# Performance work log

Measured on AMD Instinct MI355X. Metric: run time of the kernel, lower is better.

The kernel has to match this reference:

```python
import jax, jax.numpy as jnp
import numpy as np

B, C, H, W, K = 2, 3, 256, 256, 51  # output H,W; filter size K; input is (H+K-1, W+K-1)


def _sepconv(inp, vertical, horizontal):
    # inp: [B,C,H+K-1,W+K-1]; vertical/horizontal: [B,K,H,W]
    Kf = vertical.shape[1]
    Ho, Wo = vertical.shape[2], vertical.shape[3]
    rows = jnp.stack([inp[:, :, i:i + Ho, :] for i in range(Kf)], axis=0)

    def body(acc, j):
        # window for horizontal offset j: [K,B,C,Ho,Wo]
        win = jax.lax.dynamic_slice_in_dim(rows, j, Wo, axis=4)
        # contract over vertical taps i with per-pixel vertical kernel
        vcon = jnp.einsum('kbchw,bkhw->bchw', win, vertical)
        # weight by per-pixel horizontal tap j and accumulate
        acc = acc + vcon * horizontal[:, j][:, None, :, :]
        return acc, None

    acc0 = jnp.zeros((inp.shape[0], inp.shape[1], Ho, Wo), inp.dtype)
    out, _ = jax.lax.scan(body, acc0, jnp.arange(Kf))
    return out


def setup_inputs() -> dict:
    key = jax.random.key(0)
    k1, k2, k3 = jax.random.split(key, 3)
    tenInput = jax.random.normal(k1, (B, C, H + K - 1, W + K - 1), dtype=jnp.float32)
    tenVertical = jax.random.normal(k2, (B, K, H, W), dtype=jnp.float32)
    tenHorizontal = jax.random.normal(k3, (B, K, H, W), dtype=jnp.float32)
    return {"tenInput": tenInput, "tenVertical": tenVertical, "tenHorizontal": tenHorizontal}


def reference(tenInput, tenVertical, tenHorizontal):
    return _sepconv(tenInput, tenVertical, tenHorizontal)
```

## Files before the change

kernel.cpp:

```cpp
#include <hip/hip_runtime.h>


namespace {
constexpr int KK = 51;
constexpr int NB = 2;
constexpr int NC = 3;
constexpr int HH = 256;
constexpr int WW = 256;
constexpr int IN_H = HH + KK - 1;
constexpr int IN_W = WW + KK - 1;

constexpr int TILE_W = 64;
constexpr int TILE_H = 8;
constexpr int NTX = 8;
constexpr int R = 8;
constexpr int NTY = 8;
constexpr int NS = 4;
constexpr int NTHREADS = NTX * NTY * NS;
constexpr int HALO_W = TILE_W + KK - 1;
constexpr int LDS_W = 116;
constexpr int LDS_H = TILE_H + KK - 1;
constexpr int KSTRIDE = HH * WW;
}

__device__ __forceinline__ float fget(const float4 v, int i) {
  return (i == 0) ? v.x : (i == 1) ? v.y : (i == 2) ? v.z : v.w;
}

template <int P, int JJ>
__device__ __forceinline__ void fma_jtap(const float4 (&v4)[4][2], const float4 (&w4)[4][3],
                                         const float4 ha, const float4 hb, float (&acc)[R]) {
#pragma unroll
  for (int rx = 0; rx < R; ++rx) {
    const int k  = rx + JJ;
    const int sl = (P + k / 4) % 3;
    const int cp = k & 3;
    const int vh = rx >> 2, vc = rx & 3;
    float tv = fget(v4[0][vh], vc) * fget(w4[0][sl], cp);
    tv = fmaf(fget(v4[1][vh], vc), fget(w4[1][sl], cp), tv);
    tv = fmaf(fget(v4[2][vh], vc), fget(w4[2][sl], cp), tv);
    tv = fmaf(fget(v4[3][vh], vc), fget(w4[3][sl], cp), tv);
    const float hv = (rx < 4) ? fget(ha, vc) : fget(hb, vc);
    acc[rx] = fmaf(hv, tv, acc[rx]);
  }
}

template <int P>
__device__ __forceinline__ void do_chunk(const float4 (&v4)[4][2], float4 (&w4)[4][3],
                                         const int (&woff)[4], int ldcol,
                                         const float* hp, float (&acc)[R],
                                         const float* smem) {
  const float4 h0a = *reinterpret_cast<const float4*>(hp);
  const float4 h0b = *reinterpret_cast<const float4*>(hp + 4);
  const float4 h1a = *reinterpret_cast<const float4*>(hp + KSTRIDE);
  const float4 h1b = *reinterpret_cast<const float4*>(hp + KSTRIDE + 4);
  fma_jtap<P, 0>(v4, w4, h0a, h0b, acc);
  const float4 h2a = *reinterpret_cast<const float4*>(hp + 2 * (size_t)KSTRIDE);
  const float4 h2b = *reinterpret_cast<const float4*>(hp + 2 * (size_t)KSTRIDE + 4);
  const float4 h3a = *reinterpret_cast<const float4*>(hp + 3 * (size_t)KSTRIDE);
  const float4 h3b = *reinterpret_cast<const float4*>(hp + 3 * (size_t)KSTRIDE + 4);
  fma_jtap<P, 1>(v4, w4, h1a, h1b, acc);
  fma_jtap<P, 2>(v4, w4, h2a, h2b, acc);
  fma_jtap<P, 3>(v4, w4, h3a, h3b, acc);
#pragma unroll
  for (int ib = 0; ib < 4; ++ib)
    w4[ib][P] = *reinterpret_cast<const float4*>(&smem[woff[ib] + ldcol]);
}

__global__ __launch_bounds__(NTHREADS, 1)
void sepconv_kernel(
    const float* __restrict__ inp,
    const float* __restrict__ vert,
    const float* __restrict__ horiz,
    float* __restrict__ out)
{
  __shared__ float lds[LDS_H * LDS_W];

  const int tid = threadIdx.x;
  const int tx  = tid & (NTX - 1);
  const int ty  = (tid >> 3) & (NTY - 1);
  const int s   = tid >> 6;

  const int x0 = blockIdx.x * TILE_W;
  const int y0 = blockIdx.y * TILE_H;
  const int bc = blockIdx.z;
  const int b  = bc / NC;
  const int c  = bc % NC;

  {
    const float* src = inp + (((size_t)(b * NC + c)) * IN_H + y0) * IN_W + x0;
    constexpr int total2 = LDS_H * (HALO_W / 2);
    for (int e = tid; e < total2; e += NTHREADS) {
      const int col2 = e % (HALO_W / 2);
      const int r    = e / (HALO_W / 2);
      const float2 v = *reinterpret_cast<const float2*>(src + (size_t)r * IN_W + col2 * 2);
      float* dst = &lds[r * LDS_W + col2 * 2];
      dst[0] = v.x; dst[1] = v.y;
    }
  }
  __syncthreads();

  const int lx = tx * R;
  const int xg = x0 + lx;
  const int yg = y0 + ty;

  float acc[R];
#pragma unroll
  for (int rx = 0; rx < R; ++rx) acc[rx] = 0.f;

  const int blk0 = (s == 0) ? 0 : (3 * s + 1);
  const int nblk = (s == 0) ? 4 : 3;

  const float* vbase = vert  + (((size_t)b * KK) * HH + yg) * WW + xg;
  const float* hbase = horiz + (((size_t)b * KK) * HH + yg) * WW + xg;

#pragma unroll 1
  for (int t = 0; t < nblk; ++t) {
    const int ibase = (blk0 + t) * 4;

    float4 v4[4][2];
    float4 w4[4][3];
    int    woff[4];
#pragma unroll
    for (int ib = 0; ib < 4; ++ib) {
      const int iv = ibase + ib;
      const int ic = (iv <= 50) ? iv : 50;
      float4 va = *reinterpret_cast<const float4*>(vbase + (size_t)ic * KSTRIDE);
      float4 vb = *reinterpret_cast<const float4*>(vbase + (size_t)ic * KSTRIDE + 4);
      if (iv > 50) { va = make_float4(0.f, 0.f, 0.f, 0.f); vb = va; }
      v4[ib][0] = va; v4[ib][1] = vb;
      woff[ib] = (ty + ic) * LDS_W;
      const float4* p = reinterpret_cast<const float4*>(&lds[woff[ib] + lx]);
      w4[ib][0] = p[0]; w4[ib][1] = p[1]; w4[ib][2] = p[2];
    }

    const float* hp = hbase;

#pragma unroll 1
    for (int cc = 0; cc < 4; ++cc) {
      const int base = lx + 12 * cc + 12;
      do_chunk<0>(v4, w4, woff, base + 0, hp, acc, lds); hp += 4 * (size_t)KSTRIDE;
      do_chunk<1>(v4, w4, woff, base + 4, hp, acc, lds); hp += 4 * (size_t)KSTRIDE;
      do_chunk<2>(v4, w4, woff, base + 8, hp, acc, lds); hp += 4 * (size_t)KSTRIDE;
    }

    {
      const float4 e0a = *reinterpret_cast<const float4*>(hp);
      const float4 e0b = *reinterpret_cast<const float4*>(hp + 4);
      const float4 e1a = *reinterpret_cast<const float4*>(hp + KSTRIDE);
      const float4 e1b = *reinterpret_cast<const float4*>(hp + KSTRIDE + 4);
      const float4 e2a = *reinterpret_cast<const float4*>(hp + 2 * (size_t)KSTRIDE);
      const float4 e2b = *reinterpret_cast<const float4*>(hp + 2 * (size_t)KSTRIDE + 4);
      fma_jtap<0, 0>(v4, w4, e0a, e0b, acc);
      fma_jtap<0, 1>(v4, w4, e1a, e1b, acc);
      fma_jtap<0, 2>(v4, w4, e2a, e2b, acc);
    }
  }

  __syncthreads();
  if (s > 0) {
    float* p = &lds[((s - 1) * 64 + ty * NTX + tx) * R];
#pragma unroll
    for (int rx = 0; rx < R; ++rx) p[rx] = acc[rx];
  }
  __syncthreads();
  if (s == 0) {
#pragma unroll
    for (int g = 0; g < 3; ++g) {
      const float* p = &lds[(g * 64 + ty * NTX + tx) * R];
#pragma unroll
      for (int rx = 0; rx < R; ++rx) acc[rx] += p[rx];
    }
    float* o = out + (((size_t)(b * NC + c)) * HH + yg) * WW + xg;
    *reinterpret_cast<float4*>(o)     = make_float4(acc[0], acc[1], acc[2], acc[3]);
    *reinterpret_cast<float4*>(o + 4) = make_float4(acc[4], acc[5], acc[6], acc[7]);
  }
}

extern "C" void kernel_launch(void* const* d_in, const int* in_sizes, int n_in,
                              void* d_out, int out_size, void* d_ws, size_t ws_size,
                              hipStream_t stream) {
  const float* inp   = (const float*)d_in[0];
  const float* vert  = (const float*)d_in[1];
  const float* horiz = (const float*)d_in[2];
  float* out = (float*)d_out;

  dim3 grid(WW / TILE_W, HH / TILE_H, NB * NC);
  sepconv_kernel<<<grid, NTHREADS, 0, stream>>>(inp, vert, horiz, out);
}
```

Measured before the change: 159.4 us.

## Stage horizontal taps into double-buffered LDS via async global_load_lds

Instead of each of the four split-groups reading the horizontal filter taps directly from global memory (each group redundantly), the block cooperatively stages 4 taps per step into a swizzled double-buffered LDS area using global_load_lds, then all groups read from LDS. This removes the 4x redundant global reads of the horizontal weights and overlaps the next chunk's load with compute. In exchange it adds a block-wide barrier per chunk, forces all groups to iterate 4 times even when only 3 are active, and increases LDS usage.

```diff
diff --git a/kernel.cpp b/kernel.cpp
--- a/kernel.cpp
+++ b/kernel.cpp
@@ -21,6 +21,7 @@
 constexpr int LDS_W = 116;
 constexpr int LDS_H = TILE_H + KK - 1;
 constexpr int KSTRIDE = HH * WW;
+constexpr int HCH = 4 * TILE_H * TILE_W;
 }
 
 __device__ __forceinline__ float fget(const float4 v, int i) {
@@ -46,25 +47,25 @@
 }
 
 template <int P>
-__device__ __forceinline__ void do_chunk(const float4 (&v4)[4][2], float4 (&w4)[4][3],
-                                         const int (&woff)[4], int ldcol,
-                                         const float* hp, float (&acc)[R],
-                                         const float* smem) {
-  const float4 h0a = *reinterpret_cast<const float4*>(hp);
-  const float4 h0b = *reinterpret_cast<const float4*>(hp + 4);
-  const float4 h1a = *reinterpret_cast<const float4*>(hp + KSTRIDE);
-  const float4 h1b = *reinterpret_cast<const float4*>(hp + KSTRIDE + 4);
+__device__ __forceinline__ void full_chunk(const float4 (&v4)[4][2], float4 (&w4)[4][3],
+                                           const int (&woff)[4], int wcol,
+                                           const float* hb, int off0, int off1,
+                                           float (&acc)[R], const float* smem) {
+  const float4 h0a = *reinterpret_cast<const float4*>(hb + off0);
+  const float4 h0b = *reinterpret_cast<const float4*>(hb + off1);
+  const float4 h1a = *reinterpret_cast<const float4*>(hb + 512 + off0);
+  const float4 h1b = *reinterpret_cast<const float4*>(hb + 512 + off1);
   fma_jtap<P, 0>(v4, w4, h0a, h0b, acc);
-  const float4 h2a = *reinterpret_cast<const float4*>(hp + 2 * (size_t)KSTRIDE);
-  const float4 h2b = *reinterpret_cast<const float4*>(hp + 2 * (size_t)KSTRIDE + 4);
-  const float4 h3a = *reinterpret_cast<const float4*>(hp + 3 * (size_t)KSTRIDE);
-  const float4 h3b = *reinterpret_cast<const float4*>(hp + 3 * (size_t)KSTRIDE + 4);
+  const float4 h2a = *reinterpret_cast<const float4*>(hb + 1024 + off0);
+  const float4 h2b = *reinterpret_cast<const float4*>(hb + 1024 + off1);
   fma_jtap<P, 1>(v4, w4, h1a, h1b, acc);
+  const float4 h3a = *reinterpret_cast<const float4*>(hb + 1536 + off0);
+  const float4 h3b = *reinterpret_cast<const float4*>(hb + 1536 + off1);
   fma_jtap<P, 2>(v4, w4, h2a, h2b, acc);
   fma_jtap<P, 3>(v4, w4, h3a, h3b, acc);
 #pragma unroll
   for (int ib = 0; ib < 4; ++ib)
-    w4[ib][P] = *reinterpret_cast<const float4*>(&smem[woff[ib] + ldcol]);
+    w4[ib][P] = *reinterpret_cast<const float4*>(&smem[woff[ib] + wcol]);
 }
 
 __global__ __launch_bounds__(NTHREADS, 1)
@@ -75,6 +76,7 @@
     float* __restrict__ out)
 {
   __shared__ float lds[LDS_H * LDS_W];
+  __shared__ float hbuf[2 * HCH];
 
   const int tid = threadIdx.x;
   const int tx  = tid & (NTX - 1);
@@ -98,12 +100,43 @@
       dst[0] = v.x; dst[1] = v.y;
     }
   }
+
+  const float* hblk = horiz + (((size_t)b * KK) * HH + y0) * WW + x0;
+  int jj_[2], goff_[2], ldso_[2];
+#pragma unroll
+  for (int r = 0; r < 2; ++r) {
+    const int p   = r * 256 + tid;
+    const int jj  = p >> 7;
+    const int rem = p & 127;
+    const int row = rem >> 4;
+    const int c4  = rem & 15;
+    const int q   = (c4 - row) & 15;
+    jj_[r]   = jj;
+    goff_[r] = row * WW + q * 4;
+    ldso_[r] = (r * 256 + (tid & ~63)) * 4;
+  }
+  auto stage = [&](int cc, int bufn) {
+#pragma unroll
+    for (int r = 0; r < 2; ++r) {
+      const int j  = 4 * cc + jj_[r];
+      const int jc = (j <= 50) ? j : 50;
+      const float* g = hblk + (size_t)jc * KSTRIDE + goff_[r];
+      float* l = &hbuf[bufn * HCH + ldso_[r]];
+      __builtin_amdgcn_global_load_lds((const __attribute__((address_space(1))) void*)g,
+                                       (__attribute__((address_space(3))) void*)l, 16, 0, 0);
+    }
+  };
+
+  stage(0, 0);
   __syncthreads();
 
   const int lx = tx * R;
   const int xg = x0 + lx;
   const int yg = y0 + ty;
 
+  const int off0 = ty * 64 + ((2 * tx + ty) & 15) * 4;
+  const int off1 = ty * 64 + ((2 * tx + 1 + ty) & 15) * 4;
+
   float acc[R];
 #pragma unroll
   for (int rx = 0; rx < R; ++rx) acc[rx] = 0.f;
@@ -111,53 +144,62 @@
   const int blk0 = (s == 0) ? 0 : (3 * s + 1);
   const int nblk = (s == 0) ? 4 : 3;
 
-  const float* vbase = vert  + (((size_t)b * KK) * HH + yg) * WW + xg;
-  const float* hbase = horiz + (((size_t)b * KK) * HH + yg) * WW + xg;
+  const float* vbase = vert + (((size_t)b * KK) * HH + yg) * WW + xg;
+
+  int ccn = 1, buf = 0;
 
 #pragma unroll 1
-  for (int t = 0; t < nblk; ++t) {
-    const int ibase = (blk0 + t) * 4;
-
+  for (int t = 0; t < 4; ++t) {
+    const bool act = (t < nblk);
     float4 v4[4][2];
     float4 w4[4][3];
     int    woff[4];
-#pragma unroll
-    for (int ib = 0; ib < 4; ++ib) {
-      const int iv = ibase + ib;
-      const int ic = (iv <= 50) ? iv : 50;
-      float4 va = *reinterpret_cast<const float4*>(vbase + (size_t)ic * KSTRIDE);
-      float4 vb = *reinterpret_cast<const float4*>(vbase + (size_t)ic * KSTRIDE + 4);
-      if (iv > 50) { va = make_float4(0.f, 0.f, 0.f, 0.f); vb = va; }
-      v4[ib][0] = va; v4[ib][1] = vb;
-      woff[ib] = (ty + ic) * LDS_W;
-      const float4* p = reinterpret_cast<const float4*>(&lds[woff[ib] + lx]);
-      w4[ib][0] = p[0]; w4[ib][1] = p[1]; w4[ib][2] = p[2];
-    }
-
-    const float* hp = hbase;
+    if (act) {
+      const int ibase = (blk0 + t) * 4;
+#pragma unroll
+      for (int ib = 0; ib < 4; ++ib) {
+        const int iv = ibase + ib;
+        const int ic = (iv <= 50) ? iv : 50;
+        float4 va = *reinterpret_cast<const float4*>(vbase + (size_t)ic * KSTRIDE);
+        float4 vb = *reinterpret_cast<const float4*>(vbase + (size_t)ic * KSTRIDE + 4);
+        if (iv > 50) { va = make_float4(0.f, 0.f, 0.f, 0.f); vb = va; }
+        v4[ib][0] = va; v4[ib][1] = vb;
+        woff[ib] = (ty + ic) * LDS_W;
+        const float4* p = reinterpret_cast<const float4*>(&lds[woff[ib] + lx]);
+        w4[ib][0] = p[0]; w4[ib][1] = p[1]; w4[ib][2] = p[2];
+      }
+    }
 
 #pragma unroll 1
-    for (int cc = 0; cc < 4; ++cc) {
-      const int base = lx + 12 * cc + 12;
-      do_chunk<0>(v4, w4, woff, base + 0, hp, acc, lds); hp += 4 * (size_t)KSTRIDE;
-      do_chunk<1>(v4, w4, woff, base + 4, hp, acc, lds); hp += 4 * (size_t)KSTRIDE;
-      do_chunk<2>(v4, w4, woff, base + 8, hp, acc, lds); hp += 4 * (size_t)KSTRIDE;
-    }
-
-    {
-      const float4 e0a = *reinterpret_cast<const float4*>(hp);
-      const float4 e0b = *reinterpret_cast<const float4*>(hp + 4);
-      const float4 e1a = *reinterpret_cast<const float4*>(hp + KSTRIDE);
-      const float4 e1b = *reinterpret_cast<const float4*>(hp + KSTRIDE + 4);
-      const float4 e2a = *reinterpret_cast<const float4*>(hp + 2 * (size_t)KSTRIDE);
-      const float4 e2b = *reinterpret_cast<const float4*>(hp + 2 * (size_t)KSTRIDE + 4);
+    for (int g = 0; g < 4; ++g) {
+      const int base = lx + 12 * g + 12;
+      stage(ccn, buf ^ 1); ccn = (ccn == 12) ? 0 : ccn + 1;
+      if (act) full_chunk<0>(v4, w4, woff, base + 0, hbuf + buf * HCH, off0, off1, acc, lds);
+      __syncthreads(); buf ^= 1;
+      stage(ccn, buf ^ 1); ccn = (ccn == 12) ? 0 : ccn + 1;
+      if (act) full_chunk<1>(v4, w4, woff, base + 4, hbuf + buf * HCH, off0, off1, acc, lds);
+      __syncthreads(); buf ^= 1;
+      stage(ccn, buf ^ 1); ccn = (ccn == 12) ? 0 : ccn + 1;
+      if (act) full_chunk<2>(v4, w4, woff, base + 8, hbuf + buf * HCH, off0, off1, acc, lds);
+      __syncthreads(); buf ^= 1;
+    }
+
+    stage(ccn, buf ^ 1); ccn = (ccn == 12) ? 0 : ccn + 1;
+    if (act) {
+      const float* hb = hbuf + buf * HCH;
+      const float4 e0a = *reinterpret_cast<const float4*>(hb + off0);
+      const float4 e0b = *reinterpret_cast<const float4*>(hb + off1);
+      const float4 e1a = *reinterpret_cast<const float4*>(hb + 512 + off0);
+      const float4 e1b = *reinterpret_cast<const float4*>(hb + 512 + off1);
+      const float4 e2a = *reinterpret_cast<const float4*>(hb + 1024 + off0);
+      const float4 e2b = *reinterpret_cast<const float4*>(hb + 1024 + off1);
       fma_jtap<0, 0>(v4, w4, e0a, e0b, acc);
       fma_jtap<0, 1>(v4, w4, e1a, e1b, acc);
       fma_jtap<0, 2>(v4, w4, e2a, e2b, acc);
     }
-  }
-
-  __syncthreads();
+    __syncthreads(); buf ^= 1;
+  }
+
   if (s > 0) {
     float* p = &lds[((s - 1) * 64 + ty * NTX + tx) * R];
 #pragma unroll
```

After: 143.2 us. 10.1% less time.
